# Optimization experiments

Hardware: AMD Instinct MI355X
Metric: run time of the kernel (lower is better)

## Reference

```python
import jax, jax.numpy as jnp
import numpy as np

N, T, D, H = 256, 512, 256, 256


def setup_inputs() -> dict:
    key = jax.random.key(0)
    ks = jax.random.split(key, 9)
    scale_x = float(np.sqrt(6.0 / (D + H)))  # xavier_uniform range approx
    scale_h = float(np.sqrt(6.0 / (H + H)))
    def wx(k):
        return jax.random.uniform(k, (D, H), jnp.float32, -scale_x, scale_x)
    def wh(k):
        return jax.random.uniform(k, (H, H), jnp.float32, -scale_h, scale_h)
    inp = {
        'x': jax.random.normal(ks[0], (N, T, D), jnp.float32),
        'w_ii': wx(ks[1]), 'w_hi': wh(ks[2]),
        'w_if': wx(ks[3]), 'w_hf': wh(ks[4]),
        'w_ig': wx(ks[5]), 'w_hg': wh(ks[6]),
        'w_io': wx(ks[7]), 'w_ho': wh(ks[8]),
        # init_hidden() zeros all 1-D params
        'b_ii': jnp.zeros((H,), jnp.float32), 'b_hi': jnp.zeros((H,), jnp.float32),
        'b_if': jnp.zeros((H,), jnp.float32), 'b_hf': jnp.zeros((H,), jnp.float32),
        'b_ig': jnp.zeros((H,), jnp.float32), 'b_hg': jnp.zeros((H,), jnp.float32),
        'b_io': jnp.zeros((H,), jnp.float32), 'b_ho': jnp.zeros((H,), jnp.float32),
    }
    return inp


def reference(x, w_ii, w_hi, w_if, w_hf, w_ig, w_hg, w_io, w_ho,
              b_ii, b_hi, b_if, b_hf, b_ig, b_hg, b_io, b_ho):
    # Fuse the 4 input projections and 4 hidden projections into 2 GEMMs
    # (mathematically identical to the 8 separate matmuls).
    Wx = jnp.concatenate([w_ii, w_if, w_ig, w_io], axis=1)  # (D, 4H)
    Wh = jnp.concatenate([w_hi, w_hf, w_hg, w_ho], axis=1)  # (H, 4H)
    b = jnp.concatenate([b_ii + b_hi, b_if + b_hf, b_ig + b_hg, b_io + b_ho])  # (4H,)
    n, t, _ = x.shape
    h = x.shape[2]  # noqa (not used)
    # Precompute input projections for all timesteps: (T, N, 4H)
    xW = jnp.einsum('ntd,dg->tng', x, Wx)
    h0 = jnp.zeros((n, w_hi.shape[0]), x.dtype)
    c0 = jnp.zeros_like(h0)

    def step(carry, xw_t):
        h_t, c_t = carry
        gates = xw_t + h_t @ Wh + b  # (N, 4H)
        i_t, f_t, g_t, o_t = jnp.split(gates, 4, axis=1)
        i_t = jax.nn.sigmoid(i_t)
        f_t = jax.nn.sigmoid(f_t)
        g_t = jnp.tanh(g_t)
        o_t = jax.nn.sigmoid(o_t)
        c_t = f_t * c_t + i_t * g_t
        h_t = o_t * jnp.tanh(c_t)
        return (h_t, c_t), None

    (h_T, c_T), _ = jax.lax.scan(step, (h0, c0), xW)
    return (h_T, c_T)
```

## Files before the change

kernel.cpp:

```cpp
#include <hip/hip_runtime.h>
#include <cstdint>

typedef float  f32x4  __attribute__((ext_vector_type(4)));
typedef __bf16 bf16x8 __attribute__((ext_vector_type(8)));
typedef int    i32x4  __attribute__((ext_vector_type(4)));
typedef unsigned short u16;
typedef u16 u16x4 __attribute__((ext_vector_type(4)));

#define TT 512

__device__ __forceinline__ u16 f2bf(float f) {
  unsigned u = __builtin_bit_cast(unsigned, f);
  unsigned r = u + 0x7fffu + ((u >> 16) & 1u);
  return (u16)(r >> 16);
}
__device__ __forceinline__ float bflo(unsigned d) { return __builtin_bit_cast(float, d << 16); }
__device__ __forceinline__ float bfhi(unsigned d) { return __builtin_bit_cast(float, d & 0xffff0000u); }
__device__ __forceinline__ float rcpf(float x) { return __builtin_amdgcn_rcpf(x); }
__device__ __forceinline__ float fsig(float x) { return rcpf(1.f + __expf(-x)); }
__device__ __forceinline__ float ftanh(float x) { return 1.f - 2.f * rcpf(1.f + __expf(2.f * x)); }
__device__ __forceinline__ void gload_lds16(const u16* g, u16* l) {
  __builtin_amdgcn_global_load_lds((const __attribute__((address_space(1))) void*)(g),
                                   (__attribute__((address_space(3))) void*)(l), 16, 0, 0);
}

__global__ __launch_bounds__(256) void prep_w(
    const float* __restrict__ wii, const float* __restrict__ whi,
    const float* __restrict__ wif, const float* __restrict__ whf,
    const float* __restrict__ wig, const float* __restrict__ whg,
    const float* __restrict__ wio, const float* __restrict__ who,
    const float* __restrict__ bii, const float* __restrict__ bhi,
    const float* __restrict__ bif, const float* __restrict__ bhf,
    const float* __restrict__ big_, const float* __restrict__ bhg,
    const float* __restrict__ bio, const float* __restrict__ bho,
    u16* __restrict__ Wxb, signed char* __restrict__ Whq,
    float* __restrict__ wscale, float* __restrict__ bsum) {
  __shared__ float tile[64][65];
  __shared__ float red[256];
  __shared__ float scs[64];
  int b = blockIdx.x;
  int t = threadIdx.x;
  int tlo = t & 63, thi = t >> 6;

  if (b < 16) {
    const float* wx[4] = {wii, wif, wig, wio};
    int G = b >> 2, h0 = (b & 3) * 64;
    const float* src = wx[G];
    for (int dt = 0; dt < 4; ++dt) {
#pragma unroll
      for (int r = 0; r < 16; ++r) {
        int dl = r * 4 + thi;
        tile[dl][tlo] = src[(dt * 64 + dl) * 256 + h0 + tlo];
      }
      __syncthreads();
#pragma unroll
      for (int r = 0; r < 16; ++r) {
        int hl = r * 4 + thi;
        Wxb[(size_t)(G * 256 + h0 + hl) * 256 + dt * 64 + tlo] = f2bf(tile[tlo][hl]);
      }
      __syncthreads();
    }
  } else if (b < 32) {
    const float* wh[4] = {whi, whf, whg, who};
    int idx = b - 16;
    int G = idx >> 2, h0 = (idx & 3) * 64;
    const float* src = wh[G];
    float am = 0.f;
    for (int dd = 0; dd < 64; ++dd)
      am = fmaxf(am, fabsf(src[(thi * 64 + dd) * 256 + h0 + tlo]));
    red[t] = am;
    __syncthreads();
    if (t < 64) {
      float mx = fmaxf(fmaxf(red[t], red[t + 64]), fmaxf(red[t + 128], red[t + 192]));
      float scale = (mx > 0.f) ? mx * (1.f / 127.f) : 1.f;
      scs[t] = scale;
      wscale[G * 256 + h0 + t] = scale * (1.f / 127.f);
    }
    __syncthreads();
    for (int dt = 0; dt < 4; ++dt) {
#pragma unroll
      for (int r = 0; r < 16; ++r) {
        int dl = r * 4 + thi;
        tile[dl][tlo] = src[(dt * 64 + dl) * 256 + h0 + tlo];
      }
      __syncthreads();
#pragma unroll
      for (int r = 0; r < 16; ++r) {
        int hl = r * 4 + thi;
        float w = tile[tlo][hl];
        float scale = scs[hl];
        float qf = rintf(w / scale);
        qf = fminf(127.f, fmaxf(-127.f, qf));
        Whq[(size_t)(G * 256 + h0 + hl) * 256 + dt * 64 + tlo] = (signed char)(int)qf;
      }
      __syncthreads();
    }
  } else {
    const float* bx[4] = {bii, bif, big_, bio};
    const float* bh[4] = {bhi, bhf, bhg, bho};
    for (int G = 0; G < 4; ++G) bsum[G * 256 + t] = bx[G][t] + bh[G][t];
  }
}

__global__ __launch_bounds__(512, 2) void lstm_fused(
    const float* __restrict__ X, const u16* __restrict__ Bt,
    const float* __restrict__ bias, const signed char* __restrict__ Whq,
    const float* __restrict__ wscale, u16* __restrict__ xWp,
    int* __restrict__ rprog, float* __restrict__ out) {
  __shared__ u16 As[128 * 256];
  __shared__ u16 Bh[2][128 * 128];
  __shared__ __align__(16) signed char hb[2][576];
  int p = blockIdx.x;
  int tid = threadIdx.x;

  if (p >= 128) {
    int k = p - 128;
    int l = tid & 63, w8 = tid >> 6;
    int wm = w8 >> 2, wn = w8 & 3;
    int c = l & 15, q = l >> 4;
    int sw = (c & 7) << 4;
    int rowbase[4];
#pragma unroll
    for (int mt = 0; mt < 4; ++mt) rowbase[mt] = (wm * 64 + mt * 16 + c) * 512;

#define STAGE_BH(BN, HALF, BUF)                                                 \
    {                                                                           \
      _Pragma("unroll")                                                         \
      for (int s2 = 0; s2 < 4; ++s2) {                                          \
        int i = s2 * 512 + tid;                                                 \
        int cl = i >> 4, wk = i & 15;                                           \
        gload_lds16(Bt + (size_t)((BN) * 128 + cl) * 256 + (HALF) * 128 +       \
                        ((wk * 8) ^ ((cl & 7) << 3)),                           \
                    &Bh[BUF][0] + i * 8);                                       \
      }                                                                         \
    }

    for (int j = 0; j < 8; ++j) {
      int bm = j * 128 + k;
      __syncthreads();
      STAGE_BH(0, 0, 0)
#pragma unroll 4
      for (int jj = 0; jj < 16; ++jj) {
        int row_l = jj * 8 + w8;
        int d = l * 4;
        int r = bm * 128 + row_l;
        int t = r >> 8, n = r & 255;
        const float4 v = *(const float4*)(X + ((size_t)n * 512 + t) * 256 + d);
        u16x4 pk;
        pk[0] = f2bf(v.x); pk[1] = f2bf(v.y); pk[2] = f2bf(v.z); pk[3] = f2bf(v.w);
        int ba = (row_l * 512 + l * 8) ^ ((row_l & 7) << 4);
        *(u16x4*)((char*)As + ba) = pk;
      }
      __syncthreads();

      f32x4 acc[4][2];
#pragma unroll
      for (int i = 0; i < 4; ++i)
#pragma unroll
        for (int jn = 0; jn < 2; ++jn) acc[i][jn] = (f32x4){0.f, 0.f, 0.f, 0.f};

      for (int s = 0; s < 16; ++s) {
        int bn = s >> 1, half = s & 1, buf = s & 1;
        if (s < 15) {
          int sn = s + 1;
          STAGE_BH(sn >> 1, sn & 1, buf ^ 1)
        }
        const u16* bp = &Bh[buf][0];
#pragma unroll
        for (int kk = 0; kk < 4; ++kk) {
          int ko = half * 4 + kk;
          bf16x8 af[4], bfr[2];
          int koff  = (ko * 64 + q * 16) ^ sw;
          int koffb = (kk * 64 + q * 16) ^ sw;
#pragma unroll
          for (int mt = 0; mt < 4; ++mt)
            af[mt] = *(const bf16x8*)((const char*)As + rowbase[mt] + koff);
#pragma unroll
          for (int nt = 0; nt < 2; ++nt)
            bfr[nt] = *(const bf16x8*)((const char*)bp + (size_t)(wn * 32 + nt * 16 + c) * 256 + koffb);
#pragma unroll
          for (int mt = 0; mt < 4; ++mt)
#pragma unroll
            for (int nt = 0; nt < 2; ++nt)
              acc[mt][nt] = __builtin_amdgcn_mfma_f32_16x16x32_bf16(af[mt], bfr[nt], acc[mt][nt], 0, 0, 0);
        }
        if (half == 1) {
#pragma unroll
          for (int mt = 0; mt < 4; ++mt) {
            int tm = bm * 8 + wm * 4 + mt;
#pragma unroll
            for (int nt = 0; nt < 2; ++nt) {
              int tn = bn * 8 + wn * 2 + nt;
              float bv = bias[tn * 16 + c];
              u16x4 pk;
#pragma unroll
              for (int r = 0; r < 4; ++r) pk[r] = f2bf(acc[mt][nt][r] + bv);
              *reinterpret_cast<u16x4*>(xWp + ((size_t)(tm * 64 + tn) * 256 + l * 4)) = pk;
              acc[mt][nt] = (f32x4){0.f, 0.f, 0.f, 0.f};
            }
          }
        }
        __syncthreads();
      }
      if (tid == 0)
        __hip_atomic_fetch_add(&rprog[j], 1, __ATOMIC_RELEASE, __HIP_MEMORY_SCOPE_AGENT);
    }
#undef STAGE_BH
    return;
  }

  int xcd = p & 7, q8 = (p >> 3) & 7, tsel = p >> 6;
  int G = xcd * 2 + tsel;
  int wid = tid >> 6, l = tid & 63;
  int c = l & 15, q = (l >> 4) & 3;
  int tt = q >> 1, rsel = q & 1;

  for (int i = tid; i < 288; i += 512) ((int*)hb)[i] = 0;

  i32x4 bw[4][2][4];
#pragma unroll
  for (int g = 0; g < 4; ++g)
#pragma unroll
    for (int ttl = 0; ttl < 2; ++ttl) {
      int col = g * 256 + wid * 32 + ttl * 16 + c;
#pragma unroll
      for (int ks = 0; ks < 4; ++ks)
        bw[g][ttl][ks] = *reinterpret_cast<const i32x4*>(Whq + (size_t)col * 256 + ks * 64 + q * 16);
    }
  float sc8[4];
#pragma unroll
  for (int g = 0; g < 4; ++g) sc8[g] = wscale[g * 256 + wid * 32 + tt * 16 + c];

  const char* xbase = (const char*)xWp + (size_t)G * 32768;
  int xoff[4];
#pragma unroll
  for (int g = 0; g < 4; ++g) {
    int tn = g * 16 + wid * 2 + tt;
    xoff[g] = tn * 512 + (((q8 >> 1) * 16 + c) * 8) + (q8 & 1) * 4;
  }

  if (tid == 0) {
    while (__hip_atomic_load(&rprog[0], __ATOMIC_RELAXED, __HIP_MEMORY_SCOPE_AGENT) < 128)
      __builtin_amdgcn_s_sleep(8);
    (void)__hip_atomic_load(&rprog[0], __ATOMIC_ACQUIRE, __HIP_MEMORY_SCOPE_AGENT);
  }
  __syncthreads();

  unsigned xw0[4], xw1[4];
#pragma unroll
  for (int g = 0; g < 4; ++g) xw0[g] = *(const unsigned*)(xbase + xoff[g]);
  xbase += 524288;

  i32x4 zacc = (i32x4){0, 0, 0, 0};
  float cs = 0.f, hh = 0.f;
  __syncthreads();

#define STEP(CUR, XW_CUR, XW_NXT)                                               \
  {                                                                             \
    _Pragma("unroll")                                                           \
    for (int g = 0; g < 4; ++g) XW_NXT[g] = *(const unsigned*)(xbase + xoff[g]);\
    const signed char* hr = hb[CUR ^ 1];                                        \
    i32x4 acc[4][2];                                                            \
    {                                                                           \
      i32x4 a0 = *(const i32x4*)(hr + (c & 1) * 288 + q * 16);                  \
      _Pragma("unroll")                                                         \
      for (int g = 0; g < 4; ++g) {                                             \
        __asm__("v_mfma_i32_16x16x64_i8 %0, %1, %2, %3"                         \
                : "=&v"(acc[g][0]) : "v"(a0), "a"(bw[g][0][0]), "v"(zacc));     \
        __asm__("v_mfma_i32_16x16x64_i8 %0, %1, %2, %3"                         \
                : "=&v"(acc[g][1]) : "v"(a0), "a"(bw[g][1][0]), "v"(zacc));     \
      }                                                                         \
    }                                                                           \
    _Pragma("unroll")                                                           \
    for (int ks = 1; ks < 4; ++ks) {                                            \
      i32x4 a = *(const i32x4*)(hr + (c & 1) * 288 + ks * 64 + q * 16);         \
      _Pragma("unroll")                                                         \
      for (int g = 0; g < 4; ++g) {                                             \
        __asm__("v_mfma_i32_16x16x64_i8 %0, %1, %2, %0"                         \
                : "+v"(acc[g][0]) : "v"(a), "a"(bw[g][0][ks]));                 \
        __asm__("v_mfma_i32_16x16x64_i8 %0, %1, %2, %0"                         \
                : "+v"(acc[g][1]) : "v"(a), "a"(bw[g][1][ks]));                 \
      }                                                                         \
    }                                                                           \
    __asm__ volatile("s_nop 7\n\ts_nop 7\n\ts_nop 7");   \
    float a4[4];                                                                \
    _Pragma("unroll")                                                           \
    for (int g = 0; g < 4; ++g) {                                               \
      int e = tt ? (rsel ? acc[g][1][1] : acc[g][1][0])                         \
                 : (rsel ? acc[g][0][1] : acc[g][0][0]);                        \
      unsigned d = XW_CUR[g];                                                   \
      float xv = rsel ? bfhi(d) : bflo(d);                                      \
      a4[g] = (float)e * sc8[g] + xv;                                           \
    }                                                                           \
    float gi = fsig(a4[0]);                                                     \
    float gf = fsig(a4[1]);                                                     \
    float gg = ftanh(a4[2]);                                                    \
    float go = fsig(a4[3]);                                                     \
    cs = gf * cs + gi * gg;                                                     \
    hh = go * ftanh(cs);                                                        \
    int hq = (int)rintf(hh * 127.f);                                            \
    hb[CUR][rsel * 288 + wid * 32 + tt * 16 + c] = (signed char)hq;             \
    xbase += 524288;                                                            \
    __builtin_amdgcn_s_waitcnt(0xC07F);   \
    __builtin_amdgcn_s_barrier();                                               \
  }

  for (int t = 0; t < TT; t += 2) {
    STEP(0, xw0, xw1)
    if (((t + 2) & 63) == 0 && (t + 2) < TT) {
      int j = (t + 2) >> 6;
      if (tid == 0) {
        while (__hip_atomic_load(&rprog[j], __ATOMIC_RELAXED, __HIP_MEMORY_SCOPE_AGENT) < 128)
          __builtin_amdgcn_s_sleep(8);
        (void)__hip_atomic_load(&rprog[j], __ATOMIC_ACQUIRE, __HIP_MEMORY_SCOPE_AGENT);
      }
      __syncthreads();
    }
    STEP(1, xw1, xw0)
  }
#undef STEP

  {
    int n = G * 16 + q8 * 2 + rsel;
    int hu = wid * 32 + tt * 16 + c;
    out[(size_t)n * 256 + hu] = hh;
    out[65536 + (size_t)n * 256 + hu] = cs;
  }
}

extern "C" void kernel_launch(void* const* d_in, const int* in_sizes, int n_in,
                              void* d_out, int out_size, void* d_ws, size_t ws_size,
                              hipStream_t stream) {
  const float* x   = (const float*)d_in[0];
  const float* wii = (const float*)d_in[1];
  const float* whi = (const float*)d_in[2];
  const float* wif = (const float*)d_in[3];
  const float* whf = (const float*)d_in[4];
  const float* wig = (const float*)d_in[5];
  const float* whg = (const float*)d_in[6];
  const float* wio = (const float*)d_in[7];
  const float* who = (const float*)d_in[8];
  const float* bii = (const float*)d_in[9];
  const float* bhi = (const float*)d_in[10];
  const float* bif = (const float*)d_in[11];
  const float* bhf = (const float*)d_in[12];
  const float* big_ = (const float*)d_in[13];
  const float* bhg = (const float*)d_in[14];
  const float* bio = (const float*)d_in[15];
  const float* bho = (const float*)d_in[16];

  char* ws = (char*)d_ws;
  int*   rprog  = (int*)(ws);
  u16*   Wxb    = (u16*)(ws + 67108864);
  signed char* Whq = (signed char*)(ws + 67633152);
  float* wscale = (float*)(ws + 67895296);
  float* bsum   = (float*)(ws + 67899392);
  u16*   xWp    = (u16*)(ws + 67903488);
  float* out = (float*)d_out;

  hipMemsetAsync(rprog, 0, 64, stream);
  prep_w<<<33, 256, 0, stream>>>(wii, whi, wif, whf, wig, whg, wio, who,
                                 bii, bhi, bif, bhf, big_, bhg, bio, bho,
                                 Wxb, Whq, wscale, bsum);
  lstm_fused<<<256, 512, 0, stream>>>(x, Wxb, bsum, Whq, wscale, xWp, rprog, out);
}
```

Baseline: 641.1 us.

## Fuse weight prep into persistent LSTM kernel with grid-wide atomic barrier

Removes the separate prep_w launch. The 128 producer blocks now convert Wx to bf16 and quantize Wh to int8 themselves, using a wave shuffle reduction for the per-column max. A counter in rprog[8] acts as a grid barrier that both producer and recurrent blocks wait on before using the prepared weights. This saves a kernel launch and its boundary, at the cost of uncoalesced strided weight reads in each block and a spin-wait that relies on all 256 blocks being co-resident.

```diff
diff --git a/kernel.cpp b/kernel.cpp
--- a/kernel.cpp
+++ b/kernel.cpp
@@ -24,7 +24,8 @@
                                    (__attribute__((address_space(3))) void*)(l), 16, 0, 0);
 }
 
-__global__ __launch_bounds__(256) void prep_w(
+__global__ __launch_bounds__(512, 2) void lstm_fused(
+    const float* __restrict__ X,
     const float* __restrict__ wii, const float* __restrict__ whi,
     const float* __restrict__ wif, const float* __restrict__ whf,
     const float* __restrict__ wig, const float* __restrict__ whg,
@@ -34,79 +35,8 @@
     const float* __restrict__ big_, const float* __restrict__ bhg,
     const float* __restrict__ bio, const float* __restrict__ bho,
     u16* __restrict__ Wxb, signed char* __restrict__ Whq,
-    float* __restrict__ wscale, float* __restrict__ bsum) {
-  __shared__ float tile[64][65];
-  __shared__ float red[256];
-  __shared__ float scs[64];
-  int b = blockIdx.x;
-  int t = threadIdx.x;
-  int tlo = t & 63, thi = t >> 6;
-
-  if (b < 16) {
-    const float* wx[4] = {wii, wif, wig, wio};
-    int G = b >> 2, h0 = (b & 3) * 64;
-    const float* src = wx[G];
-    for (int dt = 0; dt < 4; ++dt) {
-#pragma unroll
-      for (int r = 0; r < 16; ++r) {
-        int dl = r * 4 + thi;
-        tile[dl][tlo] = src[(dt * 64 + dl) * 256 + h0 + tlo];
-      }
-      __syncthreads();
-#pragma unroll
-      for (int r = 0; r < 16; ++r) {
-        int hl = r * 4 + thi;
-        Wxb[(size_t)(G * 256 + h0 + hl) * 256 + dt * 64 + tlo] = f2bf(tile[tlo][hl]);
-      }
-      __syncthreads();
-    }
-  } else if (b < 32) {
-    const float* wh[4] = {whi, whf, whg, who};
-    int idx = b - 16;
-    int G = idx >> 2, h0 = (idx & 3) * 64;
-    const float* src = wh[G];
-    float am = 0.f;
-    for (int dd = 0; dd < 64; ++dd)
-      am = fmaxf(am, fabsf(src[(thi * 64 + dd) * 256 + h0 + tlo]));
-    red[t] = am;
-    __syncthreads();
-    if (t < 64) {
-      float mx = fmaxf(fmaxf(red[t], red[t + 64]), fmaxf(red[t + 128], red[t + 192]));
-      float scale = (mx > 0.f) ? mx * (1.f / 127.f) : 1.f;
-      scs[t] = scale;
-      wscale[G * 256 + h0 + t] = scale * (1.f / 127.f);
-    }
-    __syncthreads();
-    for (int dt = 0; dt < 4; ++dt) {
-#pragma unroll
-      for (int r = 0; r < 16; ++r) {
-        int dl = r * 4 + thi;
-        tile[dl][tlo] = src[(dt * 64 + dl) * 256 + h0 + tlo];
-      }
-      __syncthreads();
-#pragma unroll
-      for (int r = 0; r < 16; ++r) {
-        int hl = r * 4 + thi;
-        float w = tile[tlo][hl];
-        float scale = scs[hl];
-        float qf = rintf(w / scale);
-        qf = fminf(127.f, fmaxf(-127.f, qf));
-        Whq[(size_t)(G * 256 + h0 + hl) * 256 + dt * 64 + tlo] = (signed char)(int)qf;
-      }
-      __syncthreads();
-    }
-  } else {
-    const float* bx[4] = {bii, bif, big_, bio};
-    const float* bh[4] = {bhi, bhf, bhg, bho};
-    for (int G = 0; G < 4; ++G) bsum[G * 256 + t] = bx[G][t] + bh[G][t];
-  }
-}
-
-__global__ __launch_bounds__(512, 2) void lstm_fused(
-    const float* __restrict__ X, const u16* __restrict__ Bt,
-    const float* __restrict__ bias, const signed char* __restrict__ Whq,
-    const float* __restrict__ wscale, u16* __restrict__ xWp,
-    int* __restrict__ rprog, float* __restrict__ out) {
+    float* __restrict__ wscale, float* __restrict__ bsum,
+    u16* __restrict__ xWp, int* __restrict__ rprog, float* __restrict__ out) {
   __shared__ u16 As[128 * 256];
   __shared__ u16 Bh[2][128 * 128];
   __shared__ __align__(16) signed char hb[2][576];
@@ -115,6 +45,56 @@
 
   if (p >= 128) {
     int k = p - 128;
+
+    {
+      int cl = tid >> 6, dl = tid & 63;
+      int C = k * 8 + cl;
+      int G = C >> 8, h = C & 255;
+      const float* wxp[4] = {wii, wif, wig, wio};
+      const float* whp[4] = {whi, whf, whg, who};
+      const float* sx = wxp[G];
+#pragma unroll
+      for (int i = 0; i < 4; ++i) {
+        int d = i * 64 + dl;
+        Wxb[(size_t)C * 256 + d] = f2bf(sx[(size_t)d * 256 + h]);
+      }
+      const float* sh = whp[G];
+      float wv[4];
+      float am = 0.f;
+#pragma unroll
+      for (int i = 0; i < 4; ++i) {
+        int d = i * 64 + dl;
+        wv[i] = sh[(size_t)d * 256 + h];
+        am = fmaxf(am, fabsf(wv[i]));
+      }
+#pragma unroll
+      for (int off = 32; off > 0; off >>= 1)
+        am = fmaxf(am, __shfl_xor(am, off, 64));
+      float scale = (am > 0.f) ? am * (1.f / 127.f) : 1.f;
+      if (dl == 0) wscale[C] = scale * (1.f / 127.f);
+#pragma unroll
+      for (int i = 0; i < 4; ++i) {
+        float qf = rintf(wv[i] / scale);
+        qf = fminf(127.f, fmaxf(-127.f, qf));
+        Whq[(size_t)C * 256 + i * 64 + dl] = (signed char)(int)qf;
+      }
+      if (k == 0 && tid < 256) {
+        const float* bx[4] = {bii, bif, big_, bio};
+        const float* bh4[4] = {bhi, bhf, bhg, bho};
+        for (int Gg = 0; Gg < 4; ++Gg) bsum[Gg * 256 + tid] = bx[Gg][tid] + bh4[Gg][tid];
+      }
+      __syncthreads();
+      if (tid == 0)
+        __hip_atomic_fetch_add(&rprog[8], 1, __ATOMIC_RELEASE, __HIP_MEMORY_SCOPE_AGENT);
+      if (tid == 0) {
+        while (__hip_atomic_load(&rprog[8], __ATOMIC_RELAXED, __HIP_MEMORY_SCOPE_AGENT) < 128)
+          __builtin_amdgcn_s_sleep(8);
+        (void)__hip_atomic_load(&rprog[8], __ATOMIC_ACQUIRE, __HIP_MEMORY_SCOPE_AGENT);
+      }
+      __syncthreads();
+    }
+
+    const u16* Bt = Wxb;
     int l = tid & 63, w8 = tid >> 6;
     int wm = w8 >> 2, wn = w8 & 3;
     int c = l & 15, q = l >> 4;
@@ -128,9 +108,9 @@
       _Pragma("unroll")                                                         \
       for (int s2 = 0; s2 < 4; ++s2) {                                          \
         int i = s2 * 512 + tid;                                                 \
-        int cl = i >> 4, wk = i & 15;                                           \
-        gload_lds16(Bt + (size_t)((BN) * 128 + cl) * 256 + (HALF) * 128 +       \
-                        ((wk * 8) ^ ((cl & 7) << 3)),                           \
+        int cl2 = i >> 4, wk = i & 15;                                          \
+        gload_lds16(Bt + (size_t)((BN) * 128 + cl2) * 256 + (HALF) * 128 +      \
+                        ((wk * 8) ^ ((cl2 & 7) << 3)),                          \
                     &Bh[BUF][0] + i * 8);                                       \
       }                                                                         \
     }
@@ -191,7 +171,7 @@
 #pragma unroll
             for (int nt = 0; nt < 2; ++nt) {
               int tn = bn * 8 + wn * 2 + nt;
-              float bv = bias[tn * 16 + c];
+              float bv = bsum[tn * 16 + c];
               u16x4 pk;
 #pragma unroll
               for (int r = 0; r < 4; ++r) pk[r] = f2bf(acc[mt][nt][r] + bv);
@@ -216,6 +196,13 @@
   int tt = q >> 1, rsel = q & 1;
 
   for (int i = tid; i < 288; i += 512) ((int*)hb)[i] = 0;
+
+  if (tid == 0) {
+    while (__hip_atomic_load(&rprog[8], __ATOMIC_RELAXED, __HIP_MEMORY_SCOPE_AGENT) < 128)
+      __builtin_amdgcn_s_sleep(8);
+    (void)__hip_atomic_load(&rprog[8], __ATOMIC_ACQUIRE, __HIP_MEMORY_SCOPE_AGENT);
+  }
+  __syncthreads();
 
   i32x4 bw[4][2][4];
 #pragma unroll
@@ -359,8 +346,8 @@
   float* out = (float*)d_out;
 
   hipMemsetAsync(rprog, 0, 64, stream);
-  prep_w<<<33, 256, 0, stream>>>(wii, whi, wif, whf, wig, whg, wio, who,
-                                 bii, bhi, bif, bhf, big_, bhg, bio, bho,
-                                 Wxb, Whq, wscale, bsum);
-  lstm_fused<<<256, 512, 0, stream>>>(x, Wxb, bsum, Whq, wscale, xWp, rprog, out);
+  lstm_fused<<<256, 512, 0, stream>>>(x,
+                                      wii, whi, wif, whf, wig, whg, wio, who,
+                                      bii, bhi, bif, bhf, big_, bhg, bio, bho,
+                                      Wxb, Whq, wscale, bsum, xWp, rprog, out);
 }
```

After: 630.8 us. Within noise of the previous version (-1.6%).
